# Optimization experiments

Measured on AMD Instinct MI355X. Metric: run time of the kernel, lower is better.

The kernel has to match this reference:

```python
import jax, jax.numpy as jnp
import numpy as np

N_NODES = 100000
N_EDGES = 1600000
IN_DIM, HID, N_CLS = 128, 256, 40


def setup_inputs() -> dict:
    key = jax.random.key(0)
    ks = jax.random.split(key, 8)
    x = jax.random.normal(ks[0], (N_NODES, IN_DIM), dtype=jnp.float32)
    edge_index = jax.random.randint(ks[1], (2, N_EDGES), 0, N_NODES, dtype=jnp.int64)
    def glorot(k, shape):
        scale = (6.0 / (shape[0] + shape[1])) ** 0.5
        return jax.random.uniform(k, shape, jnp.float32, -scale, scale)
    return {
        "x": x,
        "edge_index": edge_index,
        "W1": glorot(ks[2], (IN_DIM, HID)),
        "b1": jnp.zeros((HID,), jnp.float32),
        "W2": glorot(ks[3], (HID, HID)),
        "b2": jnp.zeros((HID,), jnp.float32),
        "W3": glorot(ks[4], (HID, N_CLS)),
        "b3": jnp.zeros((N_CLS,), jnp.float32),
    }


def _gcn_norm(edge_index, num_nodes):
    # Add self-loops, then symmetric normalization deg^-1/2 * deg^-1/2 (PyG GCNConv).
    loops = jnp.arange(num_nodes, dtype=edge_index.dtype)
    src = jnp.concatenate([edge_index[0], loops])
    dst = jnp.concatenate([edge_index[1], loops])
    deg = jax.ops.segment_sum(jnp.ones_like(dst, dtype=jnp.float32), dst,
                              num_segments=num_nodes)
    dinv = jnp.where(deg > 0, jax.lax.rsqrt(deg), 0.0)
    norm = dinv[src] * dinv[dst]  # [E + N]
    return src, dst, norm


def _gcn_conv(x, W, b, src, dst, norm, num_nodes):
    h = x @ W                       # [N, out] dense GEMM first (out <= in here is fine)
    msg = h[src] * norm[:, None]    # irregular gather, [E+N, out]
    out = jax.ops.segment_sum(msg, dst, num_segments=num_nodes)  # scatter-add
    return out + b


def reference(x, edge_index, W1, b1, W2, b2, W3, b3):
    n = x.shape[0]
    src, dst, norm = _gcn_norm(edge_index, n)
    h = jax.nn.relu(_gcn_conv(x, W1, b1, src, dst, norm, n))
    h = jax.nn.relu(_gcn_conv(h, W2, b2, src, dst, norm, n))
    h = _gcn_conv(h, W3, b3, src, dst, norm, n)
    return jax.nn.log_softmax(h, axis=1)
```

## Files before the change

kernel.cpp:

```cpp
#include <hip/hip_runtime.h>
#include <stdint.h>
#include <math.h>

#define N_NODES 100000
#define N_EDGES 1600000
#define IN_DIM 128
#define HID 256
#define N_CLS 40
#define NBKT 391
#define NPB 391
#define BCAP 6144

typedef __attribute__((ext_vector_type(8))) short short8;
typedef __attribute__((ext_vector_type(4))) float f32x4;

__device__ __forceinline__ unsigned short f2bf(float f) {
  unsigned b = __float_as_uint(f);
  b += 0x7fffu + ((b >> 16) & 1u);
  return (unsigned short)(b >> 16);
}
__device__ __forceinline__ float bflo(unsigned u) { return __uint_as_float(u << 16); }
__device__ __forceinline__ float bfhi(unsigned u) { return __uint_as_float(u & 0xffff0000u); }

__device__ __forceinline__ int load_idx(const void* eidx, int flag, size_t pos) {
  return flag ? (int)((const long long*)eidx)[pos] : ((const int*)eidx)[pos];
}

__global__ __launch_bounds__(512) void k_pre0(const unsigned int* __restrict__ ew,
                                              int* __restrict__ flag,
                                              int* __restrict__ bucket_cursor) {
  int t = threadIdx.x;
  for (int k = t; k < NBKT; k += 512) bucket_cursor[k] = k * BCAP;
  __shared__ unsigned int sh[512];
  unsigned int v = 0;
  for (int k = t; k < 4096; k += 512) v |= ew[2 * k + 1];
  sh[t] = v;
  __syncthreads();
  for (int s = 256; s > 0; s >>= 1) {
    if (t < s) sh[t] |= sh[t + s];
    __syncthreads();
  }
  if (t == 0) flag[0] = (sh[0] == 0u) ? 1 : 0;
}

__global__ __launch_bounds__(256) void k_part(const void* __restrict__ eidx,
                                              const int* __restrict__ flagp,
                                              int* __restrict__ bucket_cursor,
                                              uint2* __restrict__ bpairs) {
  __shared__ int lcur[NBKT];
  int t = threadIdx.x;
  for (int k = t; k < NBKT; k += 256) lcur[k] = 0;
  __syncthreads();
  int flag = flagp[0];
  int base = blockIdx.x * 4096;
#pragma unroll
  for (int j = 0; j < 16; j++) {
    int e = base + j * 256 + t;
    if (e < N_EDGES) {
      int d = load_idx(eidx, flag, (size_t)N_EDGES + e);
      atomicAdd(&lcur[d >> 8], 1);
    }
  }
  __syncthreads();
  for (int k = t; k < NBKT; k += 256) {
    int c = lcur[k];
    int g = c ? atomicAdd(&bucket_cursor[k], c) : 0;
    lcur[k] = g;
  }
  __syncthreads();
#pragma unroll
  for (int j = 0; j < 16; j++) {
    int e = base + j * 256 + t;
    if (e < N_EDGES) {
      int s = load_idx(eidx, flag, e);
      int d = load_idx(eidx, flag, (size_t)N_EDGES + e);
      int p = atomicAdd(&lcur[d >> 8], 1);
      bpairs[p] = make_uint2((unsigned)s, (unsigned)d);
    }
  }
}

__global__ __launch_bounds__(256) void k_bsort(const uint2* __restrict__ bpairs,
                                               const int* __restrict__ bucket_cursor,
                                               int* __restrict__ row_start,
                                               int* __restrict__ deg,
                                               float* __restrict__ dinv,
                                               int* __restrict__ csr_src) {
  __shared__ int ldeg[256], lsum[256], lcur[256];
  int b = blockIdx.x, t = threadIdx.x;
  int d0 = b << 8;
  int nd = min(256, N_NODES - d0);
  int base = b * BCAP;
  int n = bucket_cursor[b] - base;
  ldeg[t] = 0;
  __syncthreads();
  for (int i = t; i < n; i += 256) {
    uint2 p = bpairs[base + i];
    atomicAdd(&ldeg[p.y - d0], 1);
  }
  __syncthreads();
  lsum[t] = ldeg[t];
  __syncthreads();
  for (int off = 1; off < 256; off <<= 1) {
    int v = (t >= off) ? lsum[t - off] : 0;
    __syncthreads();
    lsum[t] += v;
    __syncthreads();
  }
  int excl = lsum[t] - ldeg[t];
  if (t < nd) {
    row_start[d0 + t] = base + excl;
    deg[d0 + t] = ldeg[t];
    dinv[d0 + t] = rsqrtf((float)(ldeg[t] + 1));
  }
  lcur[t] = base + excl;
  __syncthreads();
  for (int i = t; i < n; i += 256) {
    uint2 p = bpairs[base + i];
    int pos = atomicAdd(&lcur[p.y - d0], 1);
    csr_src[pos] = (int)p.x;
  }
}

__global__ __launch_bounds__(256) void k_qxw(const float* __restrict__ x,
                                             const float* __restrict__ dinv,
                                             unsigned short* __restrict__ xq,
                                             float* __restrict__ sw_x,
                                             const float* __restrict__ W1,
                                             const float* __restrict__ W2,
                                             const float* __restrict__ W3,
                                             unsigned short* __restrict__ T1,
                                             unsigned short* __restrict__ T2,
                                             unsigned short* __restrict__ T3) {
  int b = blockIdx.x;
  if (b < 512) {
    int idx = b * 256 + threadIdx.x;
    if (idx < 32768) {
      int n = idx >> 7, k = idx & 127;
      T1[idx] = f2bf(W1[(size_t)k * HID + n]);
    } else if (idx < 98304) {
      int j = idx - 32768;
      int n = j >> 8, k = j & 255;
      T2[j] = f2bf(W2[(size_t)k * HID + n]);
    } else if (idx < 131072) {
      int j = idx - 98304;
      int n = j >> 8, k = j & 255;
      T3[j] = f2bf((n < N_CLS) ? W3[(size_t)k * N_CLS + n] : 0.f);
    }
    return;
  }
  int node = ((b - 512) << 2) + (threadIdx.x >> 6);
  int lane = threadIdx.x & 63;
  if (node >= N_NODES) return;
  float2 v = ((const float2*)x)[(size_t)node * 64 + lane];
  float m = fmaxf(fabsf(v.x), fabsf(v.y));
  for (int off = 32; off; off >>= 1) m = fmaxf(m, __shfl_down(m, off));
  m = __shfl(m, 0);
  float inv = (m > 0.f) ? 127.f / m : 0.f;
  int q0 = __float2int_rn(v.x * inv);
  int q1 = __float2int_rn(v.y * inv);
  xq[(size_t)node * 64 + lane] = (unsigned short)((q0 & 0xff) | ((q1 & 0xff) << 8));
  if (lane == 0) {
    float s = dinv[node] * ((m > 0.f) ? m / 127.f : 0.f);
    ((float2*)sw_x)[node] = make_float2(s, s);
  }
}

__device__ __forceinline__ void up4a(unsigned v, float w,
                                     float& a0, float& a1, float& a2, float& a3) {
  float f0, f1, f2, f3;
  asm("v_cvt_f32_ubyte0 %0, %1" : "=v"(f0) : "v"(v));
  asm("v_cvt_f32_ubyte1 %0, %1" : "=v"(f1) : "v"(v));
  asm("v_cvt_f32_ubyte2 %0, %1" : "=v"(f2) : "v"(v));
  asm("v_cvt_f32_ubyte3 %0, %1" : "=v"(f3) : "v"(v));
  a0 = fmaf(f0, w, a0);
  a1 = fmaf(f1, w, a1);
  a2 = fmaf(f2, w, a2);
  a3 = fmaf(f3, w, a3);
}

__global__ __launch_bounds__(256, 8) void k_agg256i(const unsigned* __restrict__ tbl,
                                                    uint2* __restrict__ out,
                                                    const float* __restrict__ dinv,
                                                    const float* __restrict__ swp,
                                                    const int* __restrict__ row_start,
                                                    const int* __restrict__ deg,
                                                    const int* __restrict__ csr_src) {
  int node = (blockIdx.x << 2) + (threadIdx.x >> 6);
  int lane = threadIdx.x & 63;
  if (node >= N_NODES) return;
  node = __builtin_amdgcn_readfirstlane(node);
  const char* tb = (const char*)tbl;
  const char* sb = (const char*)swp;
  int l4 = lane << 2;
  int h4 = (lane >= 32) ? 4 : 0;
  float d = dinv[node];
  float ws = *(const float*)(sb + ((size_t)(unsigned)node << 3) + h4);
  unsigned v0 = *(const unsigned*)(tb + ((size_t)(unsigned)node << 8) + l4);
  float a0 = 0.f, a1 = 0.f, a2 = 0.f, a3 = 0.f;

  int e0 = __builtin_amdgcn_readfirstlane(row_start[node]);
  int n = __builtin_amdgcn_readfirstlane(deg[node]);
  const int* ep = csr_src + e0;

  int idx[16];
  if (n > 0) {
#pragma unroll
    for (int j = 0; j < 16; j++) idx[j] = __builtin_amdgcn_readfirstlane(ep[min(j, n - 1)]);
  }
  up4a(v0, ws, a0, a1, a2, a3);

  int k = 0;
  for (; k + 16 <= n; k += 16) {
    int cur[16];
#pragma unroll
    for (int j = 0; j < 16; j++) cur[j] = idx[j];
    if (k + 16 < n) {
#pragma unroll
      for (int j = 0; j < 16; j++)
        idx[j] = __builtin_amdgcn_readfirstlane(ep[min(k + 16 + j, n - 1)]);
    }
    unsigned r[16];
    float w[16];
#pragma unroll
    for (int j = 0; j < 16; j++)
      r[j] = *(const unsigned*)(tb + ((size_t)(unsigned)cur[j] << 8) + l4);
#pragma unroll
    for (int j = 0; j < 16; j++)
      w[j] = *(const float*)(sb + ((size_t)(unsigned)cur[j] << 3) + h4);
#pragma unroll
    for (int j = 0; j < 16; j++) up4a(r[j], w[j], a0, a1, a2, a3);
  }
  if (k < n) {
    unsigned r[16];
    float w[16];
#pragma unroll
    for (int j = 0; j < 16; j++)
      r[j] = *(const unsigned*)(tb + ((size_t)(unsigned)idx[j] << 8) + l4);
#pragma unroll
    for (int j = 0; j < 16; j++) {
      float wv = *(const float*)(sb + ((size_t)(unsigned)idx[j] << 3) + h4);
      w[j] = (k + j < n) ? wv : 0.f;
    }
#pragma unroll
    for (int j = 0; j < 16; j++) up4a(r[j], w[j], a0, a1, a2, a3);
  }

  a0 *= d; a1 *= d; a2 *= d; a3 *= d;
  uint2 o;
  o.x = f2bf(a0) | ((unsigned)f2bf(a1) << 16);
  o.y = f2bf(a2) | ((unsigned)f2bf(a3) << 16);
  out[(size_t)node * 64 + lane] = o;
}

__global__ __launch_bounds__(256, 8) void k_agg128i(const unsigned short* __restrict__ tbl,
                                                    unsigned* __restrict__ out,
                                                    const float* __restrict__ dinv,
                                                    const float* __restrict__ sw,
                                                    const int* __restrict__ row_start,
                                                    const int* __restrict__ deg,
                                                    const int* __restrict__ csr_src) {
  int node = (blockIdx.x << 2) + (threadIdx.x >> 6);
  int lane = threadIdx.x & 63;
  if (node >= N_NODES) return;
  node = __builtin_amdgcn_readfirstlane(node);
  const char* tb = (const char*)tbl;
  const char* sb = (const char*)sw;
  int l2 = lane << 1;
  int h4 = (lane >= 32) ? 4 : 0;
  float d = dinv[node];
  float ws = *(const float*)(sb + ((size_t)(unsigned)node << 3) + h4);
  unsigned short v0 = *(const unsigned short*)(tb + ((size_t)(unsigned)node << 7) + l2);

  int e0 = __builtin_amdgcn_readfirstlane(row_start[node]);
  int n = __builtin_amdgcn_readfirstlane(deg[node]);
  const int* ep = csr_src + e0;

  int idx[16];
  if (n > 0) {
#pragma unroll
    for (int j = 0; j < 16; j++) idx[j] = __builtin_amdgcn_readfirstlane(ep[min(j, n - 1)]);
  }
  float a0 = (float)(signed char)(v0 & 0xff) * ws;
  float a1 = (float)(signed char)(v0 >> 8) * ws;

  int k = 0;
  for (; k + 16 <= n; k += 16) {
    int cur[16];
#pragma unroll
    for (int j = 0; j < 16; j++) cur[j] = idx[j];
    if (k + 16 < n) {
#pragma unroll
      for (int j = 0; j < 16; j++)
        idx[j] = __builtin_amdgcn_readfirstlane(ep[min(k + 16 + j, n - 1)]);
    }
    unsigned short r[16];
    float w[16];
#pragma unroll
    for (int j = 0; j < 16; j++)
      r[j] = *(const unsigned short*)(tb + ((size_t)(unsigned)cur[j] << 7) + l2);
#pragma unroll
    for (int j = 0; j < 16; j++)
      w[j] = *(const float*)(sb + ((size_t)(unsigned)cur[j] << 3) + h4);
#pragma unroll
    for (int j = 0; j < 16; j++) {
      a0 = fmaf((float)(signed char)(r[j] & 0xff), w[j], a0);
      a1 = fmaf((float)(signed char)(r[j] >> 8), w[j], a1);
    }
  }
  if (k < n) {
    unsigned short r[16];
    float w[16];
#pragma unroll
    for (int j = 0; j < 16; j++)
      r[j] = *(const unsigned short*)(tb + ((size_t)(unsigned)idx[j] << 7) + l2);
#pragma unroll
    for (int j = 0; j < 16; j++) {
      float wv = *(const float*)(sb + ((size_t)(unsigned)idx[j] << 3) + h4);
      w[j] = (k + j < n) ? wv : 0.f;
    }
#pragma unroll
    for (int j = 0; j < 16; j++) {
      a0 = fmaf((float)(signed char)(r[j] & 0xff), w[j], a0);
      a1 = fmaf((float)(signed char)(r[j] >> 8), w[j], a1);
    }
  }

  a0 *= d; a1 *= d;
  out[(size_t)node * 64 + lane] = f2bf(a0) | ((unsigned)f2bf(a1) << 16);
}

template<int NI>
__global__ __launch_bounds__(256) void k_gemm_bres(const unsigned short* __restrict__ A,
                                                   int lda,
                                                   const unsigned short* __restrict__ B,
                                                   const float* __restrict__ bias,
                                                   unsigned short* __restrict__ C, int ldc,
                                                   int M, int relu) {
  constexpr int BROWS = NI * 16;
  constexpr int CTS = NI * 16 + 8;
  constexpr int SMEM = (BROWS * 512 > 128 * CTS * 2) ? BROWS * 512 : 128 * CTS * 2;
  __shared__ alignas(16) char smem[SMEM];
  int tid = threadIdx.x;
  int lane = tid & 63, wv = tid >> 6;
  int quad = lane >> 4, li = lane & 15;
  int row0 = blockIdx.x * 128, col0 = blockIdx.y * (NI * 16);

  int ar0 = min(row0 + wv * 32 + li, M - 1);
  int ar1 = min(row0 + wv * 32 + 16 + li, M - 1);
  const short8* pA0 = (const short8*)(A + (size_t)ar0 * lda + quad * 8);
  const short8* pA1 = (const short8*)(A + (size_t)ar1 * lda + quad * 8);
  short8 a0 = pA0[0];
  short8 a1 = pA1[0];

  {
    const char* src = (const char*)(B + (size_t)col0 * 256);
#pragma unroll
    for (int it = 0; it < NI * 2; it++) {
      int i = tid + it * 256;
      int r = i >> 5, c = i & 31;
      *(short8*)(smem + (((r << 9) + (c << 4)) ^ ((r & 7) << 4))) =
          *(const short8*)(src + ((size_t)r << 9) + (c << 4));
    }
  }
  __syncthreads();

  f32x4 acc[2][NI];
#pragma unroll
  for (int i = 0; i < 2; i++)
#pragma unroll
    for (int j = 0; j < NI; j++) acc[i][j] = 0.f;

#pragma unroll
  for (int kc = 0; kc < 8; kc++) {
    short8 b[NI];
#pragma unroll
    for (int ni = 0; ni < NI; ni++) {
      int brow = ni * 16 + li;
      b[ni] = *(const short8*)(smem +
          (((brow << 9) + (kc << 6) + (quad << 4)) ^ ((brow & 7) << 4)));
    }
    short8 ca0 = a0, ca1 = a1;
    if (kc < 7) {
      a0 = pA0[(kc + 1) * 4];
      a1 = pA1[(kc + 1) * 4];
    }
#pragma unroll
    for (int ni = 0; ni < NI; ni++) {
      acc[0][ni] = __builtin_amdgcn_mfma_f32_16x16x32_bf16(ca0, b[ni], acc[0][ni], 0, 0, 0);
      acc[1][ni] = __builtin_amdgcn_mfma_f32_16x16x32_bf16(ca1, b[ni], acc[1][ni], 0, 0, 0);
    }
  }

  __syncthreads();
  unsigned short (*Ct)[CTS] = (unsigned short (*)[CTS])smem;
#pragma unroll
  for (int mi = 0; mi < 2; mi++)
#pragma unroll
    for (int ni = 0; ni < NI; ni++) {
      int c = ni * 16 + li;
      float bz = bias ? bias[col0 + c] : 0.f;
#pragma unroll
      for (int r = 0; r < 4; r++) {
        int row = wv * 32 + mi * 16 + quad * 4 + r;
        float o = acc[mi][ni][r] + bz;
        if (relu) o = fmaxf(o, 0.f);
        Ct[row][c] = f2bf(o);
      }
    }
  __syncthreads();
  constexpr int VC8 = NI * 2;
  constexpr int TOTAL = 128 * VC8;
#pragma unroll
  for (int it = 0; it < TOTAL / 256; it++) {
    int i = tid + it * 256;
    int row = i / VC8, ch = i % VC8;
    int gr = row0 + row;
    if (gr < M)
      *(uint4*)(C + (size_t)gr * ldc + col0 + ch * 8) = *(const uint4*)&Ct[row][ch * 8];
  }
}

__global__ __launch_bounds__(256) void k_gemm_q(const unsigned short* __restrict__ A,
                                                int lda,
                                                const unsigned short* __restrict__ B,
                                                const float* __restrict__ bias,
                                                const float* __restrict__ dinv,
                                                unsigned* __restrict__ hq,
                                                float* __restrict__ sw_h,
                                                int M) {
  __shared__ alignas(16) char smem[32768];
  int tid = threadIdx.x;
  int lane = tid & 63, wv = tid >> 6;
  int quad = lane >> 4, li = lane & 15;
  int row0 = blockIdx.x * 128, col0 = blockIdx.y * 128;
  int half = blockIdx.y;

  int ar0 = min(row0 + wv * 32 + li, M - 1);
  int ar1 = min(row0 + wv * 32 + 16 + li, M - 1);
  const short8* pA0 = (const short8*)(A + (size_t)ar0 * lda + quad * 8);
  const short8* pA1 = (const short8*)(A + (size_t)ar1 * lda + quad * 8);
  short8 a0 = pA0[0];
  short8 a1 = pA1[0];

  {
    const char* src = (const char*)(B + (size_t)col0 * 128);
#pragma unroll
    for (int it = 0; it < 8; it++) {
      int i = tid + it * 256;
      int r = i >> 4, c = i & 15;
      *(short8*)(smem + (((r << 8) + (c << 4)) ^ ((r & 7) << 4))) =
          *(const short8*)(src + ((size_t)r << 8) + (c << 4));
    }
  }
  __syncthreads();

  f32x4 acc[2][8];
#pragma unroll
  for (int i = 0; i < 2; i++)
#pragma unroll
    for (int j = 0; j < 8; j++) acc[i][j] = 0.f;

#pragma unroll
  for (int kc = 0; kc < 4; kc++) {
    short8 b[8];
#pragma unroll
    for (int ni = 0; ni < 8; ni++) {
      int brow = ni * 16 + li;
      b[ni] = *(const short8*)(smem +
          (((brow << 8) + (kc << 6) + (quad << 4)) ^ ((brow & 7) << 4)));
    }
    short8 ca0 = a0, ca1 = a1;
    if (kc < 3) {
      a0 = pA0[(kc + 1) * 4];
      a1 = pA1[(kc + 1) * 4];
    }
#pragma unroll
    for (int ni = 0; ni < 8; ni++) {
      acc[0][ni] = __builtin_amdgcn_mfma_f32_16x16x32_bf16(ca0, b[ni], acc[0][ni], 0, 0, 0);
      acc[1][ni] = __builtin_amdgcn_mfma_f32_16x16x32_bf16(ca1, b[ni], acc[1][ni], 0, 0, 0);
    }
  }

#pragma unroll
  for (int ni = 0; ni < 8; ni++) {
    float bz = bias[col0 + ni * 16 + li];
#pragma unroll
    for (int mi = 0; mi < 2; mi++)
#pragma unroll
      for (int r = 0; r < 4; r++)
        acc[mi][ni][r] = fmaxf(acc[mi][ni][r] + bz, 0.f);
  }
  float m2[2][4];
#pragma unroll
  for (int mi = 0; mi < 2; mi++)
#pragma unroll
    for (int r = 0; r < 4; r++) {
      float m = acc[mi][0][r];
#pragma unroll
      for (int ni = 1; ni < 8; ni++) m = fmaxf(m, acc[mi][ni][r]);
      m2[mi][r] = m;
    }
#pragma unroll
  for (int st = 1; st < 16; st <<= 1)
#pragma unroll
    for (int mi = 0; mi < 2; mi++)
#pragma unroll
      for (int r = 0; r < 4; r++)
        m2[mi][r] = fmaxf(m2[mi][r], __shfl_xor(m2[mi][r], st));
  float rs[2][4];
#pragma unroll
  for (int mi = 0; mi < 2; mi++)
#pragma unroll
    for (int r = 0; r < 4; r++)
      rs[mi][r] = (m2[mi][r] > 0.f) ? 255.f / m2[mi][r] : 0.f;
  if (li == 0) {
#pragma unroll
    for (int mi = 0; mi < 2; mi++)
#pragma unroll
      for (int r = 0; r < 4; r++) {
        int grow = row0 + wv * 32 + mi * 16 + quad * 4 + r;
        if (grow < M)
          sw_h[(size_t)grow * 2 + half] =
              dinv[grow] * ((m2[mi][r] > 0.f) ? m2[mi][r] / 255.f : 0.f);
      }
  }
  __syncthreads();
  unsigned char (*qtile)[128] = (unsigned char (*)[128])smem;
#pragma unroll
  for (int mi = 0; mi < 2; mi++)
#pragma unroll
    for (int ni = 0; ni < 8; ni++) {
      int c = ni * 16 + li;
#pragma unroll
      for (int r = 0; r < 4; r++) {
        int row = wv * 32 + mi * 16 + quad * 4 + r;
        qtile[row][c] = (unsigned char)__float2uint_rn(acc[mi][ni][r] * rs[mi][r]);
      }
    }
  __syncthreads();
  const uint4* qt = (const uint4*)smem;
#pragma unroll
  for (int k = 0; k < 4; k++) {
    int idx = tid + k * 256;
    int row = idx >> 3, p = idx & 7;
    int grow = row0 + row;
    if (grow < M)
      *(uint4*)(hq + (size_t)grow * 64 + half * 32 + p * 4) = qt[idx];
  }
}

__global__ __launch_bounds__(256) void k_agg40_lsm(const unsigned* __restrict__ in,
                                                   float* __restrict__ out,
                                                   const float* __restrict__ dinv,
                                                   const int* __restrict__ row_start,
                                                   const int* __restrict__ deg,
                                                   const int* __restrict__ csr_src,
                                                   const float* __restrict__ bias) {
  int node = (blockIdx.x << 2) + (threadIdx.x >> 6);
  int lane = threadIdx.x & 63;
  if (node >= N_NODES) return;
  int g = (lane >= 40) ? 2 : (lane >= 20 ? 1 : 0);
  int c = lane - g * 20;
  bool act3 = lane < 60;
  const unsigned* base = in + c;
  float d = dinv[node];
  float ws = (g == 0 && act3) ? d : 0.f;
  unsigned u0 = base[(size_t)node * 32];
  float a0 = bflo(u0) * ws, a1 = bfhi(u0) * ws;
  int eb = row_start[node];
  int e1 = eb + deg[node];
  for (; eb + 12 <= e1; eb += 12) {
    int ea = eb + g, eb2 = eb + 3 + g, ec = eb + 6 + g, ed = eb + 9 + g;
    int ia = csr_src[ea], ib = csr_src[eb2], ic = csr_src[ec], id = csr_src[ed];
    float wa = act3 ? dinv[ia] : 0.f;
    float wb = act3 ? dinv[ib] : 0.f;
    float wc = act3 ? dinv[ic] : 0.f;
    float wd = act3 ? dinv[id] : 0.f;
    unsigned ra = base[(size_t)ia * 32];
    unsigned rb = base[(size_t)ib * 32];
    unsigned rc = base[(size_t)ic * 32];
    unsigned rd = base[(size_t)id * 32];
    a0 = fmaf(bflo(ra), wa, a0); a1 = fmaf(bfhi(ra), wa, a1);
    a0 = fmaf(bflo(rb), wb, a0); a1 = fmaf(bfhi(rb), wb, a1);
    a0 = fmaf(bflo(rc), wc, a0); a1 = fmaf(bfhi(rc), wc, a1);
    a0 = fmaf(bflo(rd), wd, a0); a1 = fmaf(bfhi(rd), wd, a1);
  }
  for (; eb < e1; eb += 3) {
    int ea = eb + g;
    bool v = act3 && (ea < e1);
    int ia = v ? csr_src[ea] : 0;
    float wa = v ? dinv[ia] : 0.f;
    unsigned ra = base[(size_t)ia * 32];
    a0 = fmaf(bflo(ra), wa, a0); a1 = fmaf(bfhi(ra), wa, a1);
  }
  a0 += __shfl(a0, c + 20) + __shfl(a0, c + 40);
  a1 += __shfl(a1, c + 20) + __shfl(a1, c + 40);
  bool act = lane < 20;
  float v0 = act ? a0 * d + bias[2 * lane] : -INFINITY;
  float v1 = act ? a1 * d + bias[2 * lane + 1] : -INFINITY;
  float m = fmaxf(v0, v1);
  for (int off = 32; off; off >>= 1) m = fmaxf(m, __shfl_down(m, off));
  m = __shfl(m, 0);
  float s = act ? expf(v0 - m) + expf(v1 - m) : 0.f;
  for (int off = 32; off; off >>= 1) s += __shfl_down(s, off);
  s = __shfl(s, 0);
  float lse = m + logf(s);
  if (act) {
    out[(size_t)node * N_CLS + 2 * lane] = v0 - lse;
    out[(size_t)node * N_CLS + 2 * lane + 1] = v1 - lse;
  }
}

extern "C" void kernel_launch(void* const* d_in, const int* in_sizes, int n_in,
                              void* d_out, int out_size, void* d_ws, size_t ws_size,
                              hipStream_t stream) {
  const float* x  = (const float*)d_in[0];
  const void*  ei = d_in[1];
  const float* W1 = (const float*)d_in[2];
  const float* b1 = (const float*)d_in[3];
  const float* W2 = (const float*)d_in[4];
  const float* b2 = (const float*)d_in[5];
  const float* W3 = (const float*)d_in[6];
  const float* b3 = (const float*)d_in[7];
  float* out = (float*)d_out;

  char* w = (char*)d_ws;
  auto alloc = [&](size_t bytes) {
    char* p = w;
    w += (bytes + 255) & ~(size_t)255;
    return p;
  };
  int*   flag          = (int*)alloc(64);
  int*   bucket_cursor = (int*)alloc((size_t)NBKT * 4);
  uint2* bpairs        = (uint2*)alloc((size_t)NBKT * BCAP * 8);
  int*   csr_src       = (int*)alloc((size_t)NBKT * BCAP * 4);
  int*   row_start     = (int*)alloc((size_t)N_NODES * 4);
  int*   deg           = (int*)alloc((size_t)N_NODES * 4);
  float* dinv          = (float*)alloc((size_t)N_NODES * 4);
  float* sw_x          = (float*)alloc((size_t)N_NODES * 2 * 4);
  float* sw_h          = (float*)alloc((size_t)N_NODES * 2 * 4);
  unsigned short* Wt1  = (unsigned short*)alloc((size_t)HID * IN_DIM * 2);
  unsigned short* Wt2  = (unsigned short*)alloc((size_t)HID * HID * 2);
  unsigned short* Wt3  = (unsigned short*)alloc((size_t)128 * HID * 2);
  unsigned short* xq   = (unsigned short*)alloc((size_t)N_NODES * 64 * 2);
  unsigned*       hq   = (unsigned*)alloc((size_t)N_NODES * 64 * 4);
  char* R0 = alloc((size_t)N_NODES * HID * 2);
  char* R1 = alloc((size_t)N_NODES * HID * 2);

  unsigned*       aggX  = (unsigned*)R0;
  uint2*          aggH1 = (uint2*)R0;
  unsigned short* h2    = (unsigned short*)R1;
  unsigned short* C3    = (unsigned short*)R0;

  const int nb_w1 = (N_NODES + 3) / 4;
  const int gm    = (N_NODES + 127) / 128;

  k_pre0<<<1, 512, 0, stream>>>((const unsigned int*)ei, flag, bucket_cursor);
  k_part<<<NPB, 256, 0, stream>>>(ei, flag, bucket_cursor, bpairs);
  k_bsort<<<NBKT, 256, 0, stream>>>(bpairs, bucket_cursor, row_start, deg, dinv, csr_src);

  k_qxw<<<512 + nb_w1, 256, 0, stream>>>(x, dinv, xq, sw_x, W1, W2, W3, Wt1, Wt2, Wt3);

  k_agg128i<<<nb_w1, 256, 0, stream>>>(xq, aggX, dinv, sw_x, row_start, deg, csr_src);
  k_gemm_q<<<dim3(gm, 2), 256, 0, stream>>>((const unsigned short*)aggX, IN_DIM, Wt1, b1,
                                            dinv, hq, sw_h, N_NODES);
  k_agg256i<<<nb_w1, 256, 0, stream>>>(hq, aggH1, dinv, sw_h, row_start, deg, csr_src);
  k_gemm_bres<8><<<dim3(gm, 2), 256, 0, stream>>>((const unsigned short*)aggH1, HID, Wt2, b2,
                                                  h2, HID, N_NODES, 1);
  k_gemm_bres<4><<<dim3(gm, 1), 256, 0, stream>>>(h2, HID, Wt3, nullptr,
                                                  C3, 64, N_NODES, 0);
  k_agg40_lsm<<<nb_w1, 256, 0, stream>>>((const unsigned*)C3, out, dinv, row_start, deg,
                                         csr_src, b3);
}
```

Measured before the change: 449.1 us.

## Fuse layer-2 and layer-3 GEMMs, accumulating split-K halves with float atomics

Replaces the two back-to-back GEMM kernels (h2 = relu(aggH1·W2+b2), then h2·W3) with one kernel. Each block computes a 128-column half of h2, keeps it in shared memory, and multiplies it by the matching half of W3. The two halves are combined with float atomicAdd into a zero-initialised fp32 C3 buffer, which is cleared inside the existing prep kernel. This avoids writing and re-reading the 100000x256 bf16 h2 intermediate and drops one launch. In exchange it adds 64-wide fp32 atomic traffic, a larger shared-memory footprint, and an fp32 C3 that doubles the gather bytes in the final aggregation.

```diff
diff --git a/kernel.cpp b/kernel.cpp
--- a/kernel.cpp
+++ b/kernel.cpp
@@ -19,8 +19,6 @@
   b += 0x7fffu + ((b >> 16) & 1u);
   return (unsigned short)(b >> 16);
 }
-__device__ __forceinline__ float bflo(unsigned u) { return __uint_as_float(u << 16); }
-__device__ __forceinline__ float bfhi(unsigned u) { return __uint_as_float(u & 0xffff0000u); }
 
 __device__ __forceinline__ int load_idx(const void* eidx, int flag, size_t pos) {
   return flag ? (int)((const long long*)eidx)[pos] : ((const int*)eidx)[pos];
@@ -131,7 +129,9 @@
                                              const float* __restrict__ W3,
                                              unsigned short* __restrict__ T1,
                                              unsigned short* __restrict__ T2,
-                                             unsigned short* __restrict__ T3) {
+                                             unsigned short* __restrict__ T3,
+                                             float* __restrict__ C3f,
+                                             int nbq) {
   int b = blockIdx.x;
   if (b < 512) {
     int idx = b * 256 + threadIdx.x;
@@ -147,6 +147,11 @@
       int n = j >> 8, k = j & 255;
       T3[j] = f2bf((n < N_CLS) ? W3[(size_t)k * N_CLS + n] : 0.f);
     }
+    return;
+  }
+  if (b >= 512 + nbq) {
+    int idx = (b - 512 - nbq) * 256 + threadIdx.x;
+    if (idx < N_NODES * 16) ((float4*)C3f)[idx] = make_float4(0.f, 0.f, 0.f, 0.f);
     return;
   }
   int node = ((b - 512) << 2) + (threadIdx.x >> 6);
@@ -330,33 +335,33 @@
   out[(size_t)node * 64 + lane] = f2bf(a0) | ((unsigned)f2bf(a1) << 16);
 }
 
-template<int NI>
-__global__ __launch_bounds__(256) void k_gemm_bres(const unsigned short* __restrict__ A,
-                                                   int lda,
-                                                   const unsigned short* __restrict__ B,
-                                                   const float* __restrict__ bias,
-                                                   unsigned short* __restrict__ C, int ldc,
-                                                   int M, int relu) {
-  constexpr int BROWS = NI * 16;
-  constexpr int CTS = NI * 16 + 8;
-  constexpr int SMEM = (BROWS * 512 > 128 * CTS * 2) ? BROWS * 512 : 128 * CTS * 2;
-  __shared__ alignas(16) char smem[SMEM];
+__global__ __launch_bounds__(256) void k_gemm_fuse3(const unsigned short* __restrict__ A,
+                                                    const unsigned short* __restrict__ B,
+                                                    const unsigned short* __restrict__ W3t,
+                                                    const float* __restrict__ bias,
+                                                    float* __restrict__ C3f,
+                                                    int M) {
+  __shared__ alignas(16) char smem[65536];
+  constexpr int CTS = 136;
+  constexpr int W3OFF = 128 * CTS * 2;
   int tid = threadIdx.x;
   int lane = tid & 63, wv = tid >> 6;
   int quad = lane >> 4, li = lane & 15;
-  int row0 = blockIdx.x * 128, col0 = blockIdx.y * (NI * 16);
+  int row0 = blockIdx.x * 128;
+  int half = blockIdx.y;
+  int col0 = half * 128;
 
   int ar0 = min(row0 + wv * 32 + li, M - 1);
   int ar1 = min(row0 + wv * 32 + 16 + li, M - 1);
-  const short8* pA0 = (const short8*)(A + (size_t)ar0 * lda + quad * 8);
-  const short8* pA1 = (const short8*)(A + (size_t)ar1 * lda + quad * 8);
+  const short8* pA0 = (const short8*)(A + (size_t)ar0 * 256 + quad * 8);
+  const short8* pA1 = (const short8*)(A + (size_t)ar1 * 256 + quad * 8);
   short8 a0 = pA0[0];
   short8 a1 = pA1[0];
 
   {
     const char* src = (const char*)(B + (size_t)col0 * 256);
 #pragma unroll
-    for (int it = 0; it < NI * 2; it++) {
+    for (int it = 0; it < 16; it++) {
       int i = tid + it * 256;
       int r = i >> 5, c = i & 31;
       *(short8*)(smem + (((r << 9) + (c << 4)) ^ ((r & 7) << 4))) =
@@ -365,17 +370,17 @@
   }
   __syncthreads();
 
-  f32x4 acc[2][NI];
+  f32x4 acc[2][8];
 #pragma unroll
   for (int i = 0; i < 2; i++)
 #pragma unroll
-    for (int j = 0; j < NI; j++) acc[i][j] = 0.f;
+    for (int j = 0; j < 8; j++) acc[i][j] = 0.f;
 
 #pragma unroll
   for (int kc = 0; kc < 8; kc++) {
-    short8 b[NI];
-#pragma unroll
-    for (int ni = 0; ni < NI; ni++) {
+    short8 b[8];
+#pragma unroll
+    for (int ni = 0; ni < 8; ni++) {
       int brow = ni * 16 + li;
       b[ni] = *(const short8*)(smem +
           (((brow << 9) + (kc << 6) + (quad << 4)) ^ ((brow & 7) << 4)));
@@ -386,7 +391,7 @@
       a1 = pA1[(kc + 1) * 4];
     }
 #pragma unroll
-    for (int ni = 0; ni < NI; ni++) {
+    for (int ni = 0; ni < 8; ni++) {
       acc[0][ni] = __builtin_amdgcn_mfma_f32_16x16x32_bf16(ca0, b[ni], acc[0][ni], 0, 0, 0);
       acc[1][ni] = __builtin_amdgcn_mfma_f32_16x16x32_bf16(ca1, b[ni], acc[1][ni], 0, 0, 0);
     }
@@ -397,28 +402,66 @@
 #pragma unroll
   for (int mi = 0; mi < 2; mi++)
 #pragma unroll
-    for (int ni = 0; ni < NI; ni++) {
+    for (int ni = 0; ni < 8; ni++) {
       int c = ni * 16 + li;
-      float bz = bias ? bias[col0 + c] : 0.f;
+      float bz = bias[col0 + c];
 #pragma unroll
       for (int r = 0; r < 4; r++) {
         int row = wv * 32 + mi * 16 + quad * 4 + r;
-        float o = acc[mi][ni][r] + bz;
-        if (relu) o = fmaxf(o, 0.f);
-        Ct[row][c] = f2bf(o);
+        Ct[row][c] = f2bf(fmaxf(acc[mi][ni][r] + bz, 0.f));
       }
     }
-  __syncthreads();
-  constexpr int VC8 = NI * 2;
-  constexpr int TOTAL = 128 * VC8;
-#pragma unroll
-  for (int it = 0; it < TOTAL / 256; it++) {
-    int i = tid + it * 256;
-    int row = i / VC8, ch = i % VC8;
-    int gr = row0 + row;
-    if (gr < M)
-      *(uint4*)(C + (size_t)gr * ldc + col0 + ch * 8) = *(const uint4*)&Ct[row][ch * 8];
-  }
+  {
+    const char* src = (const char*)W3t + half * 256;
+#pragma unroll
+    for (int it = 0; it < 4; it++) {
+      int i = tid + it * 256;
+      int r = i >> 4, c = i & 15;
+      *(short8*)(smem + W3OFF + (((r << 8) + (c << 4)) ^ ((r & 7) << 4))) =
+          *(const short8*)(src + ((size_t)r << 9) + (c << 4));
+    }
+  }
+  __syncthreads();
+
+  f32x4 acc3[2][4];
+#pragma unroll
+  for (int i = 0; i < 2; i++)
+#pragma unroll
+    for (int j = 0; j < 4; j++) acc3[i][j] = 0.f;
+
+#pragma unroll
+  for (int kc = 0; kc < 4; kc++) {
+    short8 af[2];
+#pragma unroll
+    for (int mi = 0; mi < 2; mi++) {
+      int row = wv * 32 + mi * 16 + li;
+      af[mi] = *(const short8*)((const char*)smem + row * (CTS * 2) + kc * 64 + quad * 16);
+    }
+    short8 bf[4];
+#pragma unroll
+    for (int nc = 0; nc < 4; nc++) {
+      int br = nc * 16 + li;
+      bf[nc] = *(const short8*)(smem + W3OFF +
+          (((br << 8) + (kc << 6) + (quad << 4)) ^ ((br & 7) << 4)));
+    }
+#pragma unroll
+    for (int mi = 0; mi < 2; mi++)
+#pragma unroll
+      for (int nc = 0; nc < 4; nc++)
+        acc3[mi][nc] = __builtin_amdgcn_mfma_f32_16x16x32_bf16(af[mi], bf[nc], acc3[mi][nc], 0, 0, 0);
+  }
+
+#pragma unroll
+  for (int mi = 0; mi < 2; mi++)
+#pragma unroll
+    for (int nc = 0; nc < 4; nc++) {
+      int col = nc * 16 + li;
+#pragma unroll
+      for (int r = 0; r < 4; r++) {
+        int gr = row0 + wv * 32 + mi * 16 + quad * 4 + r;
+        if (gr < M) atomicAdd(&C3f[(size_t)gr * 64 + col], acc3[mi][nc][r]);
+      }
+    }
 }
 
 __global__ __launch_bounds__(256) void k_gemm_q(const unsigned short* __restrict__ A,
@@ -550,7 +593,7 @@
   }
 }
 
-__global__ __launch_bounds__(256) void k_agg40_lsm(const unsigned* __restrict__ in,
+__global__ __launch_bounds__(256) void k_agg40_lsm(const float* __restrict__ in,
                                                    float* __restrict__ out,
                                                    const float* __restrict__ dinv,
                                                    const int* __restrict__ row_start,
@@ -563,11 +606,11 @@
   int g = (lane >= 40) ? 2 : (lane >= 20 ? 1 : 0);
   int c = lane - g * 20;
   bool act3 = lane < 60;
-  const unsigned* base = in + c;
+  const float2* base = (const float2*)in + c;
   float d = dinv[node];
   float ws = (g == 0 && act3) ? d : 0.f;
-  unsigned u0 = base[(size_t)node * 32];
-  float a0 = bflo(u0) * ws, a1 = bfhi(u0) * ws;
+  float2 u0 = base[(size_t)node * 32];
+  float a0 = u0.x * ws, a1 = u0.y * ws;
   int eb = row_start[node];
   int e1 = eb + deg[node];
   for (; eb + 12 <= e1; eb += 12) {
@@ -577,22 +620,22 @@
     float wb = act3 ? dinv[ib] : 0.f;
     float wc = act3 ? dinv[ic] : 0.f;
     float wd = act3 ? dinv[id] : 0.f;
-    unsigned ra = base[(size_t)ia * 32];
-    unsigned rb = base[(size_t)ib * 32];
-    unsigned rc = base[(size_t)ic * 32];
-    unsigned rd = base[(size_t)id * 32];
-    a0 = fmaf(bflo(ra), wa, a0); a1 = fmaf(bfhi(ra), wa, a1);
-    a0 = fmaf(bflo(rb), wb, a0); a1 = fmaf(bfhi(rb), wb, a1);
-    a0 = fmaf(bflo(rc), wc, a0); a1 = fmaf(bfhi(rc), wc, a1);
-    a0 = fmaf(bflo(rd), wd, a0); a1 = fmaf(bfhi(rd), wd, a1);
+    float2 ra = base[(size_t)ia * 32];
+    float2 rb = base[(size_t)ib * 32];
+    float2 rc = base[(size_t)ic * 32];
+    float2 rd = base[(size_t)id * 32];
+    a0 = fmaf(ra.x, wa, a0); a1 = fmaf(ra.y, wa, a1);
+    a0 = fmaf(rb.x, wb, a0); a1 = fmaf(rb.y, wb, a1);
+    a0 = fmaf(rc.x, wc, a0); a1 = fmaf(rc.y, wc, a1);
+    a0 = fmaf(rd.x, wd, a0); a1 = fmaf(rd.y, wd, a1);
   }
   for (; eb < e1; eb += 3) {
     int ea = eb + g;
     bool v = act3 && (ea < e1);
     int ia = v ? csr_src[ea] : 0;
     float wa = v ? dinv[ia] : 0.f;
-    unsigned ra = base[(size_t)ia * 32];
-    a0 = fmaf(bflo(ra), wa, a0); a1 = fmaf(bfhi(ra), wa, a1);
+    float2 ra = base[(size_t)ia * 32];
+    a0 = fmaf(ra.x, wa, a0); a1 = fmaf(ra.y, wa, a1);
   }
   a0 += __shfl(a0, c + 20) + __shfl(a0, c + 40);
   a1 += __shfl(a1, c + 20) + __shfl(a1, c + 40);
@@ -646,30 +689,28 @@
   unsigned short* xq   = (unsigned short*)alloc((size_t)N_NODES * 64 * 2);
   unsigned*       hq   = (unsigned*)alloc((size_t)N_NODES * 64 * 4);
   char* R0 = alloc((size_t)N_NODES * HID * 2);
-  char* R1 = alloc((size_t)N_NODES * HID * 2);
+  float* C3f = (float*)alloc((size_t)N_NODES * 64 * 4);
 
   unsigned*       aggX  = (unsigned*)R0;
   uint2*          aggH1 = (uint2*)R0;
-  unsigned short* h2    = (unsigned short*)R1;
-  unsigned short* C3    = (unsigned short*)R0;
 
   const int nb_w1 = (N_NODES + 3) / 4;
+  const int nb_z  = (N_NODES * 16 + 255) / 256;
   const int gm    = (N_NODES + 127) / 128;
 
   k_pre0<<<1, 512, 0, stream>>>((const unsigned int*)ei, flag, bucket_cursor);
   k_part<<<NPB, 256, 0, stream>>>(ei, flag, bucket_cursor, bpairs);
   k_bsort<<<NBKT, 256, 0, stream>>>(bpairs, bucket_cursor, row_start, deg, dinv, csr_src);
 
-  k_qxw<<<512 + nb_w1, 256, 0, stream>>>(x, dinv, xq, sw_x, W1, W2, W3, Wt1, Wt2, Wt3);
+  k_qxw<<<512 + nb_w1 + nb_z, 256, 0, stream>>>(x, dinv, xq, sw_x, W1, W2, W3,
+                                                Wt1, Wt2, Wt3, C3f, nb_w1);
 
   k_agg128i<<<nb_w1, 256, 0, stream>>>(xq, aggX, dinv, sw_x, row_start, deg, csr_src);
   k_gemm_q<<<dim3(gm, 2), 256, 0, stream>>>((const unsigned short*)aggX, IN_DIM, Wt1, b1,
                                             dinv, hq, sw_h, N_NODES);
   k_agg256i<<<nb_w1, 256, 0, stream>>>(hq, aggH1, dinv, sw_h, row_start, deg, csr_src);
-  k_gemm_bres<8><<<dim3(gm, 2), 256, 0, stream>>>((const unsigned short*)aggH1, HID, Wt2, b2,
-                                                  h2, HID, N_NODES, 1);
-  k_gemm_bres<4><<<dim3(gm, 1), 256, 0, stream>>>(h2, HID, Wt3, nullptr,
-                                                  C3, 64, N_NODES, 0);
-  k_agg40_lsm<<<nb_w1, 256, 0, stream>>>((const unsigned*)C3, out, dinv, row_start, deg,
+  k_gemm_fuse3<<<dim3(gm, 2), 256, 0, stream>>>((const unsigned short*)aggH1, Wt2, Wt3,
+                                                b2, C3f, N_NODES);
+  k_agg40_lsm<<<nb_w1, 256, 0, stream>>>(C3f, out, dinv, row_start, deg,
                                          csr_src, b3);
 }
```

Measured after the change: 468.0 us. 1.04x slower.
